# Kernel tuning notes

Hardware: AMD Instinct MI355X
Metric: run time of the kernel (lower is better)

Reference implementation:

```python
import jax, jax.numpy as jnp
import numpy as np
import math

B, S, D, H, DH, R = 2, 2048, 1024, 16, 64, 8
EPS = 1e-5


def setup_inputs() -> dict:
    key = jax.random.key(0)
    ks = jax.random.split(key, 8)
    hidden_states = jax.random.normal(ks[0], (B, S, D), jnp.float32)
    # causal boolean mask (batch, seq, seq); every row has >=1 valid entry
    causal = jnp.tril(jnp.ones((S, S), dtype=bool))
    attention_mask = jnp.broadcast_to(causal, (B, S, S))
    # lora: (n_layers=1, 4, batch, hidden, rank); [0]=qA,[1]=kA,[2]=qB,[3]=kB
    lora = jax.random.normal(ks[1], (1, 4, B, D, R), jnp.float32) * 0.02
    ln_w = jnp.ones((D,), jnp.float32)
    Wq = jax.random.normal(ks[2], (D, D), jnp.float32) * 0.02
    Wk = jax.random.normal(ks[3], (D, D), jnp.float32) * 0.02
    Wv = jax.random.normal(ks[4], (D, D), jnp.float32) * 0.02
    Wo = jax.random.normal(ks[5], (D, D), jnp.float32) * 0.02
    return dict(hidden_states=hidden_states, attention_mask=attention_mask,
                lora=lora, ln_w=ln_w, Wq=Wq, Wk=Wk, Wv=Wv, Wo=Wo)


def _rms_ln(x, w):
    # model_center LayerNorm with bias=False == RMS layernorm
    var = jnp.mean(x * x, axis=-1, keepdims=True)
    return x * jax.lax.rsqrt(var + EPS) * w


def _lora_delta(h, A, Bm):
    # h: (b,s,D), A: (b,D,R), Bm: (b,R,D);  h + (h@A)@Bm * 2
    z = jnp.einsum('bsd,bdr->bsr', h, A)
    return h + jnp.einsum('bsr,brd->bsd', z, Bm) * 2


def reference(hidden_states, attention_mask, lora, ln_w, Wq, Wk, Wv, Wo):
    b, s, _ = hidden_states.shape
    x = _rms_ln(hidden_states, ln_w)
    h_q = x @ Wq.T
    h_k = x @ Wk.T
    h_v = x @ Wv.T
    layer = lora[0]  # (4, b, D, R)
    h_q = _lora_delta(h_q, layer[0], jnp.swapaxes(layer[2], 1, 2))
    h_k = _lora_delta(h_k, layer[1], jnp.swapaxes(layer[3], 1, 2))
    q = h_q.reshape(b, s, H, DH)
    k = h_k.reshape(b, s, H, DH)
    v = h_v.reshape(b, s, H, DH)
    score = jnp.einsum('bqhd,bkhd->bhqk', q, k) / math.sqrt(DH)
    m = attention_mask[:, None, :, :]  # (b,1,s,s)
    score = jnp.where(m, score, -jnp.inf)
    p = jax.nn.softmax(score, axis=-1)
    p = jnp.where(m, p, jnp.float32(0))
    out = jnp.einsum('bhqk,bkhd->bqhd', p, v).reshape(b, s, H * DH)
    out = out @ Wo.T
    return hidden_states + out
```

## Files before the change

kernel.cpp:

```cpp
#include <hip/hip_runtime.h>

typedef __bf16 bf16;
typedef __bf16 bf16x4 __attribute__((ext_vector_type(4)));
typedef __bf16 bf16x8 __attribute__((ext_vector_type(8)));
typedef float f32x4 __attribute__((ext_vector_type(4)));

#define DM 1024
#define NROW 4096
#define SEQ 2048
#define HDIM 64
#define NEGBIG -30000.0f

__device__ __forceinline__ void async16(const bf16* g, bf16* l) {
  __builtin_amdgcn_global_load_lds(
      (const __attribute__((address_space(1))) unsigned int*)g,
      (__attribute__((address_space(3))) unsigned int*)l, 16, 0, 0);
}

template <bool F32OUT>
__device__ __forceinline__ void gemm128(const bf16* __restrict__ A,
                                        const bf16* __restrict__ Bw,
                                        bf16* __restrict__ Cb,
                                        float* __restrict__ Cf,
                                        const float* __restrict__ resid,
                                        int m0, int n0) {
  __shared__ __align__(16) bf16 sA[128 * 32];
  __shared__ __align__(16) bf16 sB[128 * 32];
  const int t = threadIdx.x;
  const int lane = t & 63;
  const int w = t >> 6;
  const int wm = (w & 1) * 64;
  const int wn = (w >> 1) * 64;
  const int lr = lane & 15;
  const int kg = lane >> 4;

  f32x4 acc[4][4];
#pragma unroll
  for (int i = 0; i < 4; i++)
#pragma unroll
    for (int j = 0; j < 4; j++)
#pragma unroll
      for (int r = 0; r < 4; r++) acc[i][j][r] = 0.0f;

  const int srow = t >> 2;
  const int scol = (t & 3) * 8;
  const bf16* gA = A + (size_t)(m0 + srow) * DM + scol;
  const bf16* gB = Bw + (size_t)(n0 + srow) * DM + scol;
  bf16* lA = &sA[t * 8];
  bf16* lB = &sB[t * 8];

  for (int k0 = 0; k0 < DM; k0 += 32) {
    async16(gA + k0, lA);
    async16(gA + k0 + 64 * DM, lA + 2048);
    async16(gB + k0, lB);
    async16(gB + k0 + 64 * DM, lB + 2048);
    __syncthreads();
    bf16x8 av[4], bv[4];
#pragma unroll
    for (int mi = 0; mi < 4; mi++)
      av[mi] = *(const bf16x8*)&sA[(wm + mi * 16 + lr) * 32 + kg * 8];
#pragma unroll
    for (int nj = 0; nj < 4; nj++)
      bv[nj] = *(const bf16x8*)&sB[(wn + nj * 16 + lr) * 32 + kg * 8];
#pragma unroll
    for (int mi = 0; mi < 4; mi++)
#pragma unroll
      for (int nj = 0; nj < 4; nj++)
        acc[mi][nj] = __builtin_amdgcn_mfma_f32_16x16x32_bf16(av[mi], bv[nj],
                                                              acc[mi][nj], 0, 0, 0);
    __syncthreads();
  }

#pragma unroll
  for (int mi = 0; mi < 4; mi++) {
#pragma unroll
    for (int r = 0; r < 4; r++) {
      const int grow = m0 + wm + mi * 16 + kg * 4 + r;
      const size_t base = (size_t)grow * DM + n0 + wn + lr;
#pragma unroll
      for (int nj = 0; nj < 4; nj++) {
        float v = acc[mi][nj][r];
        if (F32OUT) {
          Cf[base + nj * 16] = v + resid[base + nj * 16];
        } else {
          Cb[base + nj * 16] = (bf16)v;
        }
      }
    }
  }
}

__global__ __launch_bounds__(256) void k_cast4(const float* __restrict__ a,
                                               const float* __restrict__ b,
                                               const float* __restrict__ c,
                                               const float* __restrict__ e,
                                               bf16* __restrict__ d) {
  const int i = blockIdx.x * 256 + threadIdx.x;
  const int mat = i >> 18;
  const int off = i & 262143;
  const float* s = (mat == 0) ? a : (mat == 1) ? b : (mat == 2) ? c : e;
  const float4 v = ((const float4*)s)[off];
  bf16x4 o;
  o[0] = (bf16)v.x; o[1] = (bf16)v.y; o[2] = (bf16)v.z; o[3] = (bf16)v.w;
  ((bf16x4*)d)[i] = o;
}

__global__ __launch_bounds__(256) void k_rmsnorm(const float* __restrict__ hin,
                                                 const float* __restrict__ wln,
                                                 bf16* __restrict__ xo) {
  const int row = blockIdx.x;
  const int t = threadIdx.x;
  const float4 h4 = ((const float4*)(hin + (size_t)row * DM))[t];
  float ss = h4.x * h4.x + h4.y * h4.y + h4.z * h4.z + h4.w * h4.w;
#pragma unroll
  for (int off = 1; off < 64; off <<= 1) ss += __shfl_xor(ss, off, 64);
  __shared__ float red[4];
  if ((t & 63) == 0) red[t >> 6] = ss;
  __syncthreads();
  ss = red[0] + red[1] + red[2] + red[3];
  const float inv = rsqrtf(ss * (1.0f / DM) + 1e-5f);
  const float4 w4 = ((const float4*)wln)[t];
  bf16x4 o;
  o[0] = (bf16)(h4.x * inv * w4.x);
  o[1] = (bf16)(h4.y * inv * w4.y);
  o[2] = (bf16)(h4.z * inv * w4.z);
  o[3] = (bf16)(h4.w * inv * w4.w);
  *(bf16x4*)&xo[(size_t)row * DM + t * 4] = o;
}

__global__ __launch_bounds__(256) void k_qkv(const bf16* __restrict__ x,
                                             const bf16* __restrict__ Wq,
                                             const bf16* __restrict__ Wk,
                                             const bf16* __restrict__ Wv,
                                             bf16* __restrict__ hq,
                                             bf16* __restrict__ hk,
                                             bf16* __restrict__ hv) {
  const int nb = blockIdx.y;
  const int wsel = nb >> 3;
  const int n0 = (nb & 7) * 128;
  const bf16* Bw = (wsel == 0) ? Wq : (wsel == 1) ? Wk : Wv;
  bf16* C = (wsel == 0) ? hq : (wsel == 1) ? hk : hv;
  gemm128<false>(x, Bw, C, nullptr, nullptr, blockIdx.x * 128, n0);
}

__global__ __launch_bounds__(256) void k_oproj(const bf16* __restrict__ ctx,
                                               const bf16* __restrict__ Wo,
                                               const float* __restrict__ resid,
                                               float* __restrict__ out) {
  gemm128<true>(ctx, Wo, nullptr, out, resid, blockIdx.x * 128, blockIdx.y * 128);
}

__global__ __launch_bounds__(256) void k_lora2(bf16* __restrict__ hq,
                                               bf16* __restrict__ hk,
                                               const float* __restrict__ lora) {
  const int row0 = blockIdx.x * 32;
  const int which = blockIdx.y;
  const int b = row0 >> 11;
  bf16* H = (which == 0 ? hq : hk) + (size_t)row0 * DM;
  const float* Am = lora + (size_t)(which == 0 ? 0 : 1) * 16384 + (size_t)b * 8192;
  const float* Bm = lora + (size_t)(which == 0 ? 2 : 3) * 16384 + (size_t)b * 8192;
  const int t = threadIdx.x;
  const int lane = t & 63;
  const int w = t >> 6;
  const int lr = lane & 15;
  const int kg = lane >> 4;

  __shared__ __align__(16) bf16 At[8 * 1024];
  __shared__ float Zp[2][32][8];

  const int d0 = lane * 16;
  float4 Bv[32];
  {
    const float4* bp = (const float4*)(Bm + (size_t)d0 * 8);
#pragma unroll
    for (int i = 0; i < 32; i++) Bv[i] = bp[i];
  }

  {
    const float4* ap = (const float4*)(Am + (size_t)t * 32);
#pragma unroll
    for (int i = 0; i < 8; i++) {
      const float4 v = ap[i];
      const int idx = t * 32 + i * 4;
      At[(idx & 7) * 1024 + (idx >> 3)]             = (bf16)v.x;
      At[((idx + 1) & 7) * 1024 + ((idx + 1) >> 3)] = (bf16)v.y;
      At[((idx + 2) & 7) * 1024 + ((idx + 2) >> 3)] = (bf16)v.z;
      At[((idx + 3) & 7) * 1024 + ((idx + 3) >> 3)] = (bf16)v.w;
    }
  }
  __syncthreads();

  const int tile = w & 1;
  const int khalf = w >> 1;
  {
    f32x4 zacc;
#pragma unroll
    for (int r = 0; r < 4; r++) zacc[r] = 0.f;
    const bf16* gH = H + (size_t)(tile * 16 + lr) * DM + khalf * 512 + kg * 8;
    const bf16* lA = &At[(lr & 7) * 1024 + khalf * 512 + kg * 8];
#pragma unroll
    for (int i = 0; i < 16; i++) {
      const bf16x8 ah = *(const bf16x8*)(gH + i * 32);
      const bf16x8 ba = *(const bf16x8*)(lA + i * 32);
      zacc = __builtin_amdgcn_mfma_f32_16x16x32_bf16(ah, ba, zacc, 0, 0, 0);
    }
    if (lr < 8) {
#pragma unroll
      for (int r = 0; r < 4; r++) Zp[khalf][tile * 16 + kg * 4 + r][lr] = zacc[r];
    }
  }
  __syncthreads();

#pragma unroll
  for (int rr = 0; rr < 8; rr++) {
    const int row = w * 8 + rr;
    const float4 z0 = *(const float4*)&Zp[0][row][0];
    const float4 z1 = *(const float4*)&Zp[0][row][4];
    const float4 y0 = *(const float4*)&Zp[1][row][0];
    const float4 y1 = *(const float4*)&Zp[1][row][4];
    const float za = z0.x + y0.x, zb = z0.y + y0.y, zc = z0.z + y0.z, zd = z0.w + y0.w;
    const float ze = z1.x + y1.x, zf = z1.y + y1.y, zg = z1.z + y1.z, zh = z1.w + y1.w;
    bf16* hp = H + (size_t)row * DM + d0;
    const bf16x8 h0 = *(const bf16x8*)hp;
    const bf16x8 h1 = *(const bf16x8*)(hp + 8);
    bf16x8 o0, o1;
#pragma unroll
    for (int j = 0; j < 16; j++) {
      const float4 b0 = Bv[2 * j];
      const float4 b1 = Bv[2 * j + 1];
      const float delta = za * b0.x + zb * b0.y + zc * b0.z + zd * b0.w +
                          ze * b1.x + zf * b1.y + zg * b1.z + zh * b1.w;
      const float hj = (j < 8) ? (float)h0[j] : (float)h1[j - 8];
      const bf16 ov = (bf16)(hj + 2.0f * delta);
      if (j < 8) o0[j] = ov; else o1[j - 8] = ov;
    }
    *(bf16x8*)hp = o0;
    *(bf16x8*)(hp + 8) = o1;
  }
}

#define PAD 72
__global__ __launch_bounds__(256, 4) void k_attn(const bf16* __restrict__ hq,
                                                 const bf16* __restrict__ hk,
                                                 const bf16* __restrict__ hv,
                                                 bf16* __restrict__ ctx) {
  const int n = blockIdx.x;
  const int slab = n & 31;
  const int hh = slab & 15;
  const int b = slab >> 4;
  const int xx = n >> 5;
  const int s = xx >> 3;
  const int v = xx & 7;
  const int qt = (s == 0) ? 4 * v : (s == 1) ? 31 - 4 * v
               : (s == 2) ? 4 * v + 2 : 29 - 4 * v;
  const int qbase = qt * 64;

  const int t = threadIdx.x;
  const int lane = t & 63;
  const int w = t >> 6;
  const int lr = lane & 15;
  const int kg = lane >> 4;

  __shared__ __align__(16) bf16 sQ[64 * PAD];
  __shared__ __align__(16) bf16 sK[64 * PAD];
  __shared__ __align__(16) bf16 sVt[64 * PAD];
  __shared__ __align__(16) bf16 sP[64 * PAD];

  const size_t rowbase = (size_t)b * SEQ;
  const int hoff = hh * HDIM;
  const float sscale = 0.18033688011112042f;

  {
    const int r = t >> 2;
    const int c0 = (t & 3) * 16;
    const bf16* g = hq + (rowbase + qbase + r) * DM + hoff + c0;
    bf16x8 q0 = *(const bf16x8*)g;
    bf16x8 q1 = *(const bf16x8*)(g + 8);
    bf16x8 o0, o1;
#pragma unroll
    for (int j = 0; j < 8; j++) {
      o0[j] = (bf16)((float)q0[j] * sscale);
      o1[j] = (bf16)((float)q1[j] * sscale);
    }
    *(bf16x8*)&sQ[r * PAD + c0] = o0;
    *(bf16x8*)&sQ[r * PAD + c0 + 8] = o1;
  }

  const int rK = t >> 2;
  const int cK = (t & 3) * 16;
  const bf16* gK = hk + (rowbase + rK) * DM + hoff + cK;
  const bf16* gV = hv + (rowbase + lane) * DM + hoff + w * 16;
  bf16x8 kr0 = *(const bf16x8*)gK;
  bf16x8 kr1 = *(const bf16x8*)(gK + 8);
  bf16x8 vr0 = *(const bf16x8*)gV;
  bf16x8 vr1 = *(const bf16x8*)(gV + 8);

  float m_l = NEGBIG, l_l = 0.f;
  f32x4 oacc[4];
#pragma unroll
  for (int nj = 0; nj < 4; nj++)
#pragma unroll
    for (int r = 0; r < 4; r++) oacc[nj][r] = 0.f;

  __syncthreads();

  for (int kt = 0; kt <= qt; kt++) {
    *(bf16x8*)&sK[rK * PAD + cK] = kr0;
    *(bf16x8*)&sK[rK * PAD + cK + 8] = kr1;
    {
      const int c0 = w * 16;
#pragma unroll
      for (int j = 0; j < 8; j++) {
        sVt[(c0 + j) * PAD + lane] = vr0[j];
        sVt[(c0 + 8 + j) * PAD + lane] = vr1[j];
      }
    }
    __syncthreads();

    if (kt < qt) {
      const bf16* gK2 = gK + (size_t)(kt + 1) * 64 * DM;
      const bf16* gV2 = gV + (size_t)(kt + 1) * 64 * DM;
      kr0 = *(const bf16x8*)gK2;
      kr1 = *(const bf16x8*)(gK2 + 8);
      vr0 = *(const bf16x8*)gV2;
      vr1 = *(const bf16x8*)(gV2 + 8);
    }

    f32x4 sc[4];
#pragma unroll
    for (int nj = 0; nj < 4; nj++)
#pragma unroll
      for (int r = 0; r < 4; r++) sc[nj][r] = 0.f;
#pragma unroll
    for (int ks = 0; ks < 2; ks++) {
      const bf16x8 bq = *(const bf16x8*)&sQ[(w * 16 + lr) * PAD + ks * 32 + kg * 8];
#pragma unroll
      for (int nj = 0; nj < 4; nj++) {
        const bf16x8 ak = *(const bf16x8*)&sK[(nj * 16 + lr) * PAD + ks * 32 + kg * 8];
        sc[nj] = __builtin_amdgcn_mfma_f32_16x16x32_bf16(ak, bq, sc[nj], 0, 0, 0);
      }
    }

    if (kt == qt) {
      const int ql = w * 16 + lr;
#pragma unroll
      for (int nj = 0; nj < 4; nj++)
#pragma unroll
        for (int r = 0; r < 4; r++) {
          const int kl = nj * 16 + kg * 4 + r;
          sc[nj][r] = (kl <= ql) ? sc[nj][r] : NEGBIG;
        }
    }

    float rm = sc[0][0];
#pragma unroll
    for (int nj = 0; nj < 4; nj++)
#pragma unroll
      for (int r = 0; r < 4; r++) rm = fmaxf(rm, sc[nj][r]);
    rm = fmaxf(rm, __shfl_xor(rm, 16, 64));
    rm = fmaxf(rm, __shfl_xor(rm, 32, 64));
    const float mnew = fmaxf(m_l, rm);
    const float alpha = __builtin_amdgcn_exp2f(m_l - mnew);
    float rs = 0.f;
#pragma unroll
    for (int nj = 0; nj < 4; nj++)
#pragma unroll
      for (int r = 0; r < 4; r++) {
        const float p = __builtin_amdgcn_exp2f(sc[nj][r] - mnew);
        sc[nj][r] = p;
        rs += p;
      }
    rs += __shfl_xor(rs, 16, 64);
    rs += __shfl_xor(rs, 32, 64);
    l_l = l_l * alpha + rs;
    m_l = mnew;

#pragma unroll
    for (int nj = 0; nj < 4; nj++)
#pragma unroll
      for (int r = 0; r < 4; r++)
        sP[(w * 16 + lr) * PAD + nj * 16 + kg * 4 + r] = (bf16)sc[nj][r];

#pragma unroll
    for (int r = 0; r < 4; r++) {
      const float ar = __shfl(alpha, (lane & 48) | (kg * 4 + r), 64);
#pragma unroll
      for (int nj = 0; nj < 4; nj++) oacc[nj][r] *= ar;
    }

#pragma unroll
    for (int ks = 0; ks < 2; ks++) {
      const bf16x8 ap = *(const bf16x8*)&sP[(w * 16 + lr) * PAD + ks * 32 + kg * 8];
#pragma unroll
      for (int nj = 0; nj < 4; nj++) {
        const bf16x8 bv = *(const bf16x8*)&sVt[(nj * 16 + lr) * PAD + ks * 32 + kg * 8];
        oacc[nj] = __builtin_amdgcn_mfma_f32_16x16x32_bf16(ap, bv, oacc[nj], 0, 0, 0);
      }
    }
    __syncthreads();
  }

#pragma unroll
  for (int r = 0; r < 4; r++) {
    const float lrow = __shfl(l_l, (lane & 48) | (kg * 4 + r), 64);
    const float invl = 1.0f / lrow;
    const int qr = qbase + w * 16 + kg * 4 + r;
    const size_t base = (rowbase + qr) * DM + hoff + lr;
#pragma unroll
    for (int nj = 0; nj < 4; nj++)
      ctx[base + nj * 16] = (bf16)(oacc[nj][r] * invl);
  }
}

extern "C" void kernel_launch(void* const* d_in, const int* in_sizes, int n_in,
                              void* d_out, int out_size, void* d_ws, size_t ws_size,
                              hipStream_t stream) {
  const float* hidden = (const float*)d_in[0];
  const float* lora = (const float*)d_in[2];
  const float* wln  = (const float*)d_in[3];
  const float* Wq   = (const float*)d_in[4];
  const float* Wk   = (const float*)d_in[5];
  const float* Wv   = (const float*)d_in[6];
  const float* Wo   = (const float*)d_in[7];
  float* out = (float*)d_out;

  const size_t BUF = (size_t)NROW * DM;
  if (ws_size < 4 * BUF * sizeof(bf16)) return;
  bf16* ws = (bf16*)d_ws;
  bf16* hq  = ws;
  bf16* hk  = ws + 1 * BUF;
  bf16* hv  = ws + 2 * BUF;
  bf16* ctx = ws + 3 * BUF;

  bf16* dob = (bf16*)d_out;
  bf16* x   = dob;
  bf16* wqb = dob + BUF;
  bf16* wkb = dob + BUF + DM * DM;
  bf16* wvb = dob + BUF + 2 * DM * DM;
  bf16* wob = dob + BUF + 3 * DM * DM;

  k_cast4<<<dim3(4 * 1024), dim3(256), 0, stream>>>(Wq, Wk, Wv, Wo, wqb);
  k_rmsnorm<<<dim3(NROW), dim3(256), 0, stream>>>(hidden, wln, x);
  k_qkv<<<dim3(32, 24), dim3(256), 0, stream>>>(x, wqb, wkb, wvb, hq, hk, hv);
  k_lora2<<<dim3(128, 2), dim3(256), 0, stream>>>(hq, hk, lora);
  k_attn<<<dim3(1024), dim3(256), 0, stream>>>(hq, hk, hv, ctx);
  k_oproj<<<dim3(32, 8), dim3(256), 0, stream>>>(ctx, wob, hidden, out);
}
```

Baseline: 228.5 us.

## Restructure attention into 32-row query tiles with register-held K fragments

The attention kernel now runs 128-thread blocks, each handling two paired 32-row query tiles (p and 63-p) to balance causal work. Q and K MFMA fragments are loaded straight from global memory into registers, so the shared-memory Q and K staging is gone. V is transposed into double-buffered shared memory with packed 32-bit writes, and P is staged per wave. The Wo cast moves into its own kernel that runs after attention and writes into the freed hq buffer. The aim is to cut LDS traffic and barriers, at the cost of more redundant global K loads per block and lower per-block parallelism.

```diff
diff --git a/kernel.cpp b/kernel.cpp
--- a/kernel.cpp
+++ b/kernel.cpp
@@ -90,16 +90,24 @@
   }
 }
 
-__global__ __launch_bounds__(256) void k_cast4(const float* __restrict__ a,
+__global__ __launch_bounds__(256) void k_cast3(const float* __restrict__ a,
                                                const float* __restrict__ b,
                                                const float* __restrict__ c,
-                                               const float* __restrict__ e,
                                                bf16* __restrict__ d) {
   const int i = blockIdx.x * 256 + threadIdx.x;
   const int mat = i >> 18;
   const int off = i & 262143;
-  const float* s = (mat == 0) ? a : (mat == 1) ? b : (mat == 2) ? c : e;
+  const float* s = (mat == 0) ? a : (mat == 1) ? b : c;
   const float4 v = ((const float4*)s)[off];
+  bf16x4 o;
+  o[0] = (bf16)v.x; o[1] = (bf16)v.y; o[2] = (bf16)v.z; o[3] = (bf16)v.w;
+  ((bf16x4*)d)[i] = o;
+}
+
+__global__ __launch_bounds__(256) void k_cast(const float* __restrict__ s,
+                                              bf16* __restrict__ d) {
+  const int i = blockIdx.x * 256 + threadIdx.x;
+  const float4 v = ((const float4*)s)[i];
   bf16x4 o;
   o[0] = (bf16)v.x; o[1] = (bf16)v.y; o[2] = (bf16)v.z; o[3] = (bf16)v.w;
   ((bf16x4*)d)[i] = o;
@@ -239,8 +247,8 @@
   }
 }
 
-#define PAD 72
-__global__ __launch_bounds__(256, 4) void k_attn(const bf16* __restrict__ hq,
+#define PADV 72
+__global__ __launch_bounds__(128, 2) void k_attn(const bf16* __restrict__ hq,
                                                  const bf16* __restrict__ hk,
                                                  const bf16* __restrict__ hv,
                                                  bf16* __restrict__ ctx) {
@@ -248,167 +256,177 @@
   const int slab = n & 31;
   const int hh = slab & 15;
   const int b = slab >> 4;
-  const int xx = n >> 5;
-  const int s = xx >> 3;
-  const int v = xx & 7;
-  const int qt = (s == 0) ? 4 * v : (s == 1) ? 31 - 4 * v
-               : (s == 2) ? 4 * v + 2 : 29 - 4 * v;
-  const int qbase = qt * 64;
-
+  const int p = n >> 5;
   const int t = threadIdx.x;
   const int lane = t & 63;
   const int w = t >> 6;
   const int lr = lane & 15;
   const int kg = lane >> 4;
 
-  __shared__ __align__(16) bf16 sQ[64 * PAD];
-  __shared__ __align__(16) bf16 sK[64 * PAD];
-  __shared__ __align__(16) bf16 sVt[64 * PAD];
-  __shared__ __align__(16) bf16 sP[64 * PAD];
+  __shared__ __align__(16) bf16 sVt[2][64 * PADV];
+  __shared__ __align__(16) bf16 sP[2][16 * PADV];
 
   const size_t rowbase = (size_t)b * SEQ;
   const int hoff = hh * HDIM;
   const float sscale = 0.18033688011112042f;
 
-  {
-    const int r = t >> 2;
-    const int c0 = (t & 3) * 16;
-    const bf16* g = hq + (rowbase + qbase + r) * DM + hoff + c0;
-    bf16x8 q0 = *(const bf16x8*)g;
-    bf16x8 q1 = *(const bf16x8*)(g + 8);
-    bf16x8 o0, o1;
-#pragma unroll
-    for (int j = 0; j < 8; j++) {
-      o0[j] = (bf16)((float)q0[j] * sscale);
-      o1[j] = (bf16)((float)q1[j] * sscale);
-    }
-    *(bf16x8*)&sQ[r * PAD + c0] = o0;
-    *(bf16x8*)&sQ[r * PAD + c0 + 8] = o1;
-  }
-
-  const int rK = t >> 2;
-  const int cK = (t & 3) * 16;
-  const bf16* gK = hk + (rowbase + rK) * DM + hoff + cK;
-  const bf16* gV = hv + (rowbase + lane) * DM + hoff + w * 16;
-  bf16x8 kr0 = *(const bf16x8*)gK;
-  bf16x8 kr1 = *(const bf16x8*)(gK + 8);
-  bf16x8 vr0 = *(const bf16x8*)gV;
-  bf16x8 vr1 = *(const bf16x8*)(gV + 8);
-
-  float m_l = NEGBIG, l_l = 0.f;
-  f32x4 oacc[4];
-#pragma unroll
-  for (int nj = 0; nj < 4; nj++)
-#pragma unroll
-    for (int r = 0; r < 4; r++) oacc[nj][r] = 0.f;
-
-  __syncthreads();
-
-  for (int kt = 0; kt <= qt; kt++) {
-    *(bf16x8*)&sK[rK * PAD + cK] = kr0;
-    *(bf16x8*)&sK[rK * PAD + cK + 8] = kr1;
+  const int vrow = 2 * (t & 31);
+  const int vcol = (t >> 5) * 16;
+  const bf16* vb = hv + (rowbase + vrow) * DM + hoff + vcol;
+  const bf16* kb = hk + (rowbase + lr) * DM + hoff + kg * 8;
+
+  int pp = 0;
+
+#pragma unroll 1
+  for (int sub = 0; sub < 2; sub++) {
+    const int qt = sub ? (63 - p) : p;
+    const int qbase = qt * 32;
+    const int nkt = (qt >> 1) + 1;
+
+    bf16x8 bq[2];
     {
-      const int c0 = w * 16;
-#pragma unroll
-      for (int j = 0; j < 8; j++) {
-        sVt[(c0 + j) * PAD + lane] = vr0[j];
-        sVt[(c0 + 8 + j) * PAD + lane] = vr1[j];
-      }
-    }
-    __syncthreads();
-
-    if (kt < qt) {
-      const bf16* gK2 = gK + (size_t)(kt + 1) * 64 * DM;
-      const bf16* gV2 = gV + (size_t)(kt + 1) * 64 * DM;
-      kr0 = *(const bf16x8*)gK2;
-      kr1 = *(const bf16x8*)(gK2 + 8);
-      vr0 = *(const bf16x8*)gV2;
-      vr1 = *(const bf16x8*)(gV2 + 8);
-    }
-
-    f32x4 sc[4];
+      const bf16* gq = hq + (rowbase + qbase + w * 16 + lr) * DM + hoff;
+#pragma unroll
+      for (int ks = 0; ks < 2; ks++) {
+        const bf16x8 raw = *(const bf16x8*)(gq + ks * 32 + kg * 8);
+#pragma unroll
+        for (int j = 0; j < 8; j++) bq[ks][j] = (bf16)((float)raw[j] * sscale);
+      }
+    }
+
+    bf16x8 vr0 = *(const bf16x8*)vb;
+    bf16x8 vr1 = *(const bf16x8*)(vb + 8);
+    bf16x8 vr2 = *(const bf16x8*)(vb + DM);
+    bf16x8 vr3 = *(const bf16x8*)(vb + DM + 8);
+    bf16x8 kr[4][2];
 #pragma unroll
     for (int nj = 0; nj < 4; nj++)
 #pragma unroll
-      for (int r = 0; r < 4; r++) sc[nj][r] = 0.f;
-#pragma unroll
-    for (int ks = 0; ks < 2; ks++) {
-      const bf16x8 bq = *(const bf16x8*)&sQ[(w * 16 + lr) * PAD + ks * 32 + kg * 8];
-#pragma unroll
-      for (int nj = 0; nj < 4; nj++) {
-        const bf16x8 ak = *(const bf16x8*)&sK[(nj * 16 + lr) * PAD + ks * 32 + kg * 8];
-        sc[nj] = __builtin_amdgcn_mfma_f32_16x16x32_bf16(ak, bq, sc[nj], 0, 0, 0);
-      }
-    }
-
-    if (kt == qt) {
-      const int ql = w * 16 + lr;
+      for (int ks = 0; ks < 2; ks++)
+        kr[nj][ks] = *(const bf16x8*)(kb + (size_t)(nj * 16) * DM + ks * 32);
+
+    float m_l = NEGBIG, l_l = 0.f;
+    f32x4 oacc[4];
+#pragma unroll
+    for (int nj = 0; nj < 4; nj++)
+#pragma unroll
+      for (int r = 0; r < 4; r++) oacc[nj][r] = 0.f;
+
+#pragma unroll 1
+    for (int kt = 0; kt < nkt; kt++) {
+      const int buf = pp & 1;
+      pp++;
+
+      {
+        const unsigned short* e0 = (const unsigned short*)&vr0;
+        const unsigned short* e1 = (const unsigned short*)&vr1;
+        const unsigned short* e2 = (const unsigned short*)&vr2;
+        const unsigned short* e3 = (const unsigned short*)&vr3;
+        bf16* base = &sVt[buf][0];
+#pragma unroll
+        for (int c = 0; c < 8; c++) {
+          *(unsigned int*)&base[(vcol + c) * PADV + vrow] =
+              ((unsigned int)e2[c] << 16) | e0[c];
+          *(unsigned int*)&base[(vcol + 8 + c) * PADV + vrow] =
+              ((unsigned int)e3[c] << 16) | e1[c];
+        }
+      }
+      __syncthreads();
+
+      f32x4 sc[4];
+#pragma unroll
+      for (int nj = 0; nj < 4; nj++)
+#pragma unroll
+        for (int r = 0; r < 4; r++) sc[nj][r] = 0.f;
+#pragma unroll
+      for (int ks = 0; ks < 2; ks++)
+#pragma unroll
+        for (int nj = 0; nj < 4; nj++)
+          sc[nj] = __builtin_amdgcn_mfma_f32_16x16x32_bf16(kr[nj][ks], bq[ks],
+                                                           sc[nj], 0, 0, 0);
+
+      if (kt + 1 < nkt) {
+        const size_t koff = (size_t)(kt + 1) * 64 * DM;
+        vr0 = *(const bf16x8*)(vb + koff);
+        vr1 = *(const bf16x8*)(vb + koff + 8);
+        vr2 = *(const bf16x8*)(vb + koff + DM);
+        vr3 = *(const bf16x8*)(vb + koff + DM + 8);
+#pragma unroll
+        for (int nj = 0; nj < 4; nj++)
+#pragma unroll
+          for (int ks = 0; ks < 2; ks++)
+            kr[nj][ks] = *(const bf16x8*)(kb + koff + (size_t)(nj * 16) * DM + ks * 32);
+      }
+
+      if (kt == nkt - 1) {
+        const int thr = 32 * (qt & 1) + w * 16 + lr;
+#pragma unroll
+        for (int nj = 0; nj < 4; nj++)
+#pragma unroll
+          for (int r = 0; r < 4; r++) {
+            const int kl = nj * 16 + kg * 4 + r;
+            sc[nj][r] = (kl <= thr) ? sc[nj][r] : NEGBIG;
+          }
+      }
+
+      float rm = sc[0][0];
+#pragma unroll
+      for (int nj = 0; nj < 4; nj++)
+#pragma unroll
+        for (int r = 0; r < 4; r++) rm = fmaxf(rm, sc[nj][r]);
+      rm = fmaxf(rm, __shfl_xor(rm, 16, 64));
+      rm = fmaxf(rm, __shfl_xor(rm, 32, 64));
+      const float mnew = fmaxf(m_l, rm);
+      const float alpha = __builtin_amdgcn_exp2f(m_l - mnew);
+      float rs = 0.f;
 #pragma unroll
       for (int nj = 0; nj < 4; nj++)
 #pragma unroll
         for (int r = 0; r < 4; r++) {
-          const int kl = nj * 16 + kg * 4 + r;
-          sc[nj][r] = (kl <= ql) ? sc[nj][r] : NEGBIG;
+          const float pv = __builtin_amdgcn_exp2f(sc[nj][r] - mnew);
+          sc[nj][r] = pv;
+          rs += pv;
         }
-    }
-
-    float rm = sc[0][0];
-#pragma unroll
-    for (int nj = 0; nj < 4; nj++)
-#pragma unroll
-      for (int r = 0; r < 4; r++) rm = fmaxf(rm, sc[nj][r]);
-    rm = fmaxf(rm, __shfl_xor(rm, 16, 64));
-    rm = fmaxf(rm, __shfl_xor(rm, 32, 64));
-    const float mnew = fmaxf(m_l, rm);
-    const float alpha = __builtin_amdgcn_exp2f(m_l - mnew);
-    float rs = 0.f;
-#pragma unroll
-    for (int nj = 0; nj < 4; nj++)
+      rs += __shfl_xor(rs, 16, 64);
+      rs += __shfl_xor(rs, 32, 64);
+      l_l = l_l * alpha + rs;
+      m_l = mnew;
+
+#pragma unroll
+      for (int nj = 0; nj < 4; nj++)
+#pragma unroll
+        for (int r = 0; r < 4; r++)
+          sP[w][lr * PADV + nj * 16 + kg * 4 + r] = (bf16)sc[nj][r];
+
 #pragma unroll
       for (int r = 0; r < 4; r++) {
-        const float p = __builtin_amdgcn_exp2f(sc[nj][r] - mnew);
-        sc[nj][r] = p;
-        rs += p;
-      }
-    rs += __shfl_xor(rs, 16, 64);
-    rs += __shfl_xor(rs, 32, 64);
-    l_l = l_l * alpha + rs;
-    m_l = mnew;
-
-#pragma unroll
-    for (int nj = 0; nj < 4; nj++)
-#pragma unroll
-      for (int r = 0; r < 4; r++)
-        sP[(w * 16 + lr) * PAD + nj * 16 + kg * 4 + r] = (bf16)sc[nj][r];
+        const float ar = __shfl(alpha, (lane & 48) | (kg * 4 + r), 64);
+#pragma unroll
+        for (int nj = 0; nj < 4; nj++) oacc[nj][r] *= ar;
+      }
+
+#pragma unroll
+      for (int ks = 0; ks < 2; ks++) {
+        const bf16x8 ap = *(const bf16x8*)&sP[w][lr * PADV + ks * 32 + kg * 8];
+#pragma unroll
+        for (int nj = 0; nj < 4; nj++) {
+          const bf16x8 bv = *(const bf16x8*)&sVt[buf][(nj * 16 + lr) * PADV + ks * 32 + kg * 8];
+          oacc[nj] = __builtin_amdgcn_mfma_f32_16x16x32_bf16(ap, bv, oacc[nj], 0, 0, 0);
+        }
+      }
+      __syncthreads();
+    }
 
 #pragma unroll
     for (int r = 0; r < 4; r++) {
-      const float ar = __shfl(alpha, (lane & 48) | (kg * 4 + r), 64);
-#pragma unroll
-      for (int nj = 0; nj < 4; nj++) oacc[nj][r] *= ar;
-    }
-
-#pragma unroll
-    for (int ks = 0; ks < 2; ks++) {
-      const bf16x8 ap = *(const bf16x8*)&sP[(w * 16 + lr) * PAD + ks * 32 + kg * 8];
-#pragma unroll
-      for (int nj = 0; nj < 4; nj++) {
-        const bf16x8 bv = *(const bf16x8*)&sVt[(nj * 16 + lr) * PAD + ks * 32 + kg * 8];
-        oacc[nj] = __builtin_amdgcn_mfma_f32_16x16x32_bf16(ap, bv, oacc[nj], 0, 0, 0);
-      }
-    }
-    __syncthreads();
-  }
-
-#pragma unroll
-  for (int r = 0; r < 4; r++) {
-    const float lrow = __shfl(l_l, (lane & 48) | (kg * 4 + r), 64);
-    const float invl = 1.0f / lrow;
-    const int qr = qbase + w * 16 + kg * 4 + r;
-    const size_t base = (rowbase + qr) * DM + hoff + lr;
-#pragma unroll
-    for (int nj = 0; nj < 4; nj++)
-      ctx[base + nj * 16] = (bf16)(oacc[nj][r] * invl);
+      const float lrow = __shfl(l_l, (lane & 48) | (kg * 4 + r), 64);
+      const float invl = 1.0f / lrow;
+      const int qr = qbase + w * 16 + kg * 4 + r;
+      const size_t base = (rowbase + qr) * DM + hoff + lr;
+#pragma unroll
+      for (int nj = 0; nj < 4; nj++)
+        ctx[base + nj * 16] = (bf16)(oacc[nj][r] * invl);
+    }
   }
 }
 
@@ -437,12 +455,13 @@
   bf16* wqb = dob + BUF;
   bf16* wkb = dob + BUF + DM * DM;
   bf16* wvb = dob + BUF + 2 * DM * DM;
-  bf16* wob = dob + BUF + 3 * DM * DM;
-
-  k_cast4<<<dim3(4 * 1024), dim3(256), 0, stream>>>(Wq, Wk, Wv, Wo, wqb);
+  bf16* wob = hq;
+
+  k_cast3<<<dim3(3 * 1024), dim3(256), 0, stream>>>(Wq, Wk, Wv, wqb);
   k_rmsnorm<<<dim3(NROW), dim3(256), 0, stream>>>(hidden, wln, x);
   k_qkv<<<dim3(32, 24), dim3(256), 0, stream>>>(x, wqb, wkb, wvb, hq, hk, hv);
   k_lora2<<<dim3(128, 2), dim3(256), 0, stream>>>(hq, hk, lora);
-  k_attn<<<dim3(1024), dim3(256), 0, stream>>>(hq, hk, hv, ctx);
+  k_attn<<<dim3(1024), dim3(128), 0, stream>>>(hq, hk, hv, ctx);
+  k_cast<<<dim3(1024), dim3(256), 0, stream>>>(Wo, wob);
   k_oproj<<<dim3(32, 8), dim3(256), 0, stream>>>(ctx, wob, hidden, out);
 }
```

Result: slower. 271.9 us (+19.0%).
